# Performance work log

Hardware: AMD Instinct MI355X
Metric: run time of the kernel (lower is better)

## Reference

```python
import jax, jax.numpy as jnp
jax.config.update("jax_enable_x64", True)  # hash needs int64 wraparound semantics like torch
import numpy as np

HASH_BITS = 19
HASH_SIZE = 1 << HASH_BITS   # 2**hash_size entries
CELL_SIZE = 1.0
DIM = 8                      # feature dimensions
N = 8_388_608                # number of query positions


def _bitmix_hash(ix, iy):
    """Murmur-inspired bit-mix hash, int64 wraparound arithmetic (matches torch .long())."""
    h = ix
    h = h ^ (h >> 16)
    h = h * jnp.int64(2246822507)
    h = h ^ (h >> 13)
    h = h + iy * jnp.int64(3266489909)
    h = h ^ (h >> 16)
    return jnp.mod(h, HASH_SIZE)  # nonneg result, same as torch/python %


def setup_inputs() -> dict:
    key = jax.random.key(0)
    k1, k2 = jax.random.split(key)
    positions = jax.random.uniform(k1, (N, 2), dtype=jnp.float32, minval=0.0, maxval=4096.0)
    # dense materialization of the lazily-inserted ParameterDict: randn * 0.01 init
    table = jax.random.normal(k2, (HASH_SIZE, DIM), dtype=jnp.float32) * 0.01
    return {"positions": positions, "table": table}


def reference(positions, table):
    # quantize to integer grid cells
    ix = jnp.floor(positions[:, 0] / CELL_SIZE).astype(jnp.int64)
    iy = jnp.floor(positions[:, 1] / CELL_SIZE).astype(jnp.int64)
    idx = _bitmix_hash(ix, iy)          # [N] in [0, HASH_SIZE)
    return jnp.take(table, idx, axis=0)  # [N, DIM] gather
```

## Files before the change

kernel.cpp:

```cpp
#include <hip/hip_runtime.h>
#include <stdint.h>

#define HASH_BITS 19
#define HASH_SIZE (1u << HASH_BITS)

#define SLICE_BITS 3
#define NSLICE (1 << SLICE_BITS)
#define SLICE_SHIFT (HASH_BITS - SLICE_BITS)

#define BLOCK 256
#define IPT 8
#define CHUNK (BLOCK * IPT)

typedef float vfloat2 __attribute__((ext_vector_type(2)));
typedef float vfloat4 __attribute__((ext_vector_type(4)));

__device__ __forceinline__ uint32_t bitmix_hash(float qx, float qy) {
    uint64_t ix = (uint64_t)(uint32_t)qx;
    uint64_t iy = (uint64_t)(uint32_t)qy;
    uint64_t hh = ix;
    hh ^= hh >> 16;
    hh *= 2246822507ull;
    hh ^= hh >> 13;
    hh += iy * 3266489909ull;
    hh ^= hh >> 16;
    return (uint32_t)hh & (HASH_SIZE - 1);
}

__global__ __launch_bounds__(BLOCK) void hashgrid2d_phased(
    const vfloat2* __restrict__ pos,
    const vfloat4* __restrict__ table,
    vfloat4* __restrict__ out,
    int n, int nchunks)
{
    __shared__ vfloat4 vals[CHUNK * 2];
    const int t = threadIdx.x;

    for (int c = blockIdx.x; c < nchunks; c += gridDim.x) {
        const long long base = (long long)c * CHUNK;

        uint32_t idx[IPT];
#pragma unroll
        for (int j = 0; j < IPT; ++j) {
            long long g = base + j * BLOCK + t;
            if (g < n) {
                vfloat2 q = __builtin_nontemporal_load(&pos[g]);
                idx[j] = bitmix_hash(q.x, q.y);
            } else {
                idx[j] = 0xFFFFFFFFu;
            }
        }

        __syncthreads();

#pragma unroll 1
        for (uint32_t s = 0; s < NSLICE; ++s) {
#pragma unroll
            for (int j = 0; j < IPT; ++j) {
                if ((idx[j] >> SLICE_SHIFT) == s) {
                    size_t e = (size_t)idx[j] * 2;
                    vfloat4 lo = table[e];
                    vfloat4 hi = table[e + 1];
                    int li = j * BLOCK + t;
                    vals[li * 2]     = lo;
                    vals[li * 2 + 1] = hi;
                }
            }
        }

        __syncthreads();

#pragma unroll
        for (int k = 0; k < IPT * 2; ++k) {
            int f = k * BLOCK + t;
            long long item = base + (f >> 1);
            if (item < n)
                __builtin_nontemporal_store(vals[f], &out[base * 2 + f]);
        }
    }
}

extern "C" void kernel_launch(void* const* d_in, const int* in_sizes, int n_in,
                              void* d_out, int out_size, void* d_ws, size_t ws_size,
                              hipStream_t stream) {
    const vfloat2* pos   = (const vfloat2*)d_in[0];
    const vfloat4* table = (const vfloat4*)d_in[1];
    vfloat4* out         = (vfloat4*)d_out;

    int n = in_sizes[0] / 2;
    int nchunks = (int)(((long long)n + CHUNK - 1) / CHUNK);
    int grid = nchunks < 512 ? nchunks : 512;
    hashgrid2d_phased<<<grid, BLOCK, 0, stream>>>(pos, table, out, n, nchunks);
}
```

Before: 495.5 us.

## Split into bucketing pass and per-slice gather pass via workspace records

Replaces the single phased kernel with two kernels. The first hashes positions and uses ballot-based counting sort to write packed (local id, hash index) records grouped by table slice per 8K-item group. The second launches one block per (group, slice) so that concurrently running blocks touch limited table regions. The aim is better cache locality for the random table gather. In exchange it adds a workspace round trip for the records, a second launch, scattered output stores, and a fallback kernel for when the workspace is too small.

```diff
diff --git a/kernel.cpp b/kernel.cpp
--- a/kernel.cpp
+++ b/kernel.cpp
@@ -3,14 +3,13 @@
 
 #define HASH_BITS 19
 #define HASH_SIZE (1u << HASH_BITS)
+#define SLICE_SHIFT (HASH_BITS - 3)
+#define NSLICE 8
 
-#define SLICE_BITS 3
-#define NSLICE (1 << SLICE_BITS)
-#define SLICE_SHIFT (HASH_BITS - SLICE_BITS)
-
+#define GROUP_BITS 13
+#define GROUP (1 << GROUP_BITS)
 #define BLOCK 256
-#define IPT 8
-#define CHUNK (BLOCK * IPT)
+#define IPT (GROUP / BLOCK)
 
 typedef float vfloat2 __attribute__((ext_vector_type(2)));
 typedef float vfloat4 __attribute__((ext_vector_type(4)));
@@ -27,56 +26,124 @@
     return (uint32_t)hh & (HASH_SIZE - 1);
 }
 
-__global__ __launch_bounds__(BLOCK) void hashgrid2d_phased(
+__global__ __launch_bounds__(BLOCK) void bucket_kernel(
+    const vfloat2* __restrict__ pos,
+    uint32_t* __restrict__ records,
+    uint32_t* __restrict__ hdr,
+    long long n)
+{
+    __shared__ uint32_t cnt[BLOCK / 64][NSLICE];
+    __shared__ uint32_t scan[BLOCK / 64][NSLICE];
+    const int g = blockIdx.x;
+    const long long gbase = (long long)g << GROUP_BITS;
+    const int tid = threadIdx.x;
+    const int w = tid >> 6;
+    const int lane = tid & 63;
+    const uint64_t lt_mask = (lane == 63) ? ~0ull >> 1 : ((1ull << (lane + 1)) >> 1) - 0;
+    const uint64_t lt = (lane == 0) ? 0ull : (~0ull >> (64 - lane));
+    (void)lt_mask;
+
+    uint32_t idx[IPT];
+#pragma unroll
+    for (int j = 0; j < IPT; ++j) {
+        long long item = gbase + j * BLOCK + tid;
+        if (item < n) {
+            vfloat2 q = __builtin_nontemporal_load(&pos[item]);
+            idx[j] = bitmix_hash(q.x, q.y);
+        } else {
+            idx[j] = 0xFFFFFFFFu;
+        }
+    }
+
+    uint32_t c[NSLICE] = {0, 0, 0, 0, 0, 0, 0, 0};
+#pragma unroll
+    for (int j = 0; j < IPT; ++j) {
+        uint32_t sl = idx[j] >> SLICE_SHIFT;
+#pragma unroll
+        for (uint32_t s0 = 0; s0 < NSLICE; ++s0)
+            c[s0] += (uint32_t)__popcll(__ballot(sl == s0));
+    }
+    if (lane == 0) {
+#pragma unroll
+        for (int s0 = 0; s0 < NSLICE; ++s0) cnt[w][s0] = c[s0];
+    }
+    __syncthreads();
+
+    if (tid == 0) {
+        uint32_t run = 0;
+        for (int s0 = 0; s0 < NSLICE; ++s0) {
+            hdr[(size_t)g * NSLICE + s0] = run;
+            for (int w0 = 0; w0 < BLOCK / 64; ++w0) {
+                scan[w0][s0] = run;
+                run += cnt[w0][s0];
+            }
+        }
+    }
+    __syncthreads();
+
+    uint32_t off[NSLICE];
+#pragma unroll
+    for (int s0 = 0; s0 < NSLICE; ++s0) off[s0] = scan[w][s0];
+
+#pragma unroll
+    for (int j = 0; j < IPT; ++j) {
+        uint32_t sl = idx[j] >> SLICE_SHIFT;
+        uint32_t lid = (uint32_t)(j * BLOCK + tid);
+#pragma unroll
+        for (uint32_t s0 = 0; s0 < NSLICE; ++s0) {
+            uint64_t m = __ballot(sl == s0);
+            if (sl == s0) {
+                uint32_t rank = (uint32_t)__popcll(m & lt);
+                records[gbase + off[s0] + rank] = (lid << HASH_BITS) | idx[j];
+            }
+            off[s0] += (uint32_t)__popcll(m);
+        }
+    }
+}
+
+__global__ __launch_bounds__(BLOCK) void gather_kernel(
+    const uint32_t* __restrict__ records,
+    const uint32_t* __restrict__ hdr,
+    const vfloat4* __restrict__ table,
+    vfloat4* __restrict__ out,
+    long long n)
+{
+    const uint32_t s = blockIdx.x & (NSLICE - 1);
+    const uint32_t g = blockIdx.x >> 3;
+    const long long gbase = (long long)g << GROUP_BITS;
+    long long rem = n - gbase;
+    uint32_t gvalid = rem >= GROUP ? (uint32_t)GROUP : (uint32_t)rem;
+    uint32_t b = hdr[(size_t)g * NSLICE + s];
+    uint32_t e = (s == NSLICE - 1) ? gvalid : hdr[(size_t)g * NSLICE + s + 1];
+
+    for (uint32_t i = threadIdx.x + b; i < e; i += BLOCK) {
+        uint32_t rec = __builtin_nontemporal_load(&records[gbase + i]);
+        uint32_t id = rec & (HASH_SIZE - 1);
+        uint32_t lid = rec >> HASH_BITS;
+        vfloat4 lo = table[(size_t)id * 2];
+        vfloat4 hi = table[(size_t)id * 2 + 1];
+        size_t o = (size_t)(gbase + lid) * 2;
+        __builtin_nontemporal_store(lo, &out[o]);
+        __builtin_nontemporal_store(hi, &out[o + 1]);
+    }
+}
+
+__global__ __launch_bounds__(256) void hashgrid2d_fallback(
     const vfloat2* __restrict__ pos,
     const vfloat4* __restrict__ table,
     vfloat4* __restrict__ out,
-    int n, int nchunks)
+    long long n)
 {
-    __shared__ vfloat4 vals[CHUNK * 2];
-    const int t = threadIdx.x;
-
-    for (int c = blockIdx.x; c < nchunks; c += gridDim.x) {
-        const long long base = (long long)c * CHUNK;
-
-        uint32_t idx[IPT];
-#pragma unroll
-        for (int j = 0; j < IPT; ++j) {
-            long long g = base + j * BLOCK + t;
-            if (g < n) {
-                vfloat2 q = __builtin_nontemporal_load(&pos[g]);
-                idx[j] = bitmix_hash(q.x, q.y);
-            } else {
-                idx[j] = 0xFFFFFFFFu;
-            }
-        }
-
-        __syncthreads();
-
-#pragma unroll 1
-        for (uint32_t s = 0; s < NSLICE; ++s) {
-#pragma unroll
-            for (int j = 0; j < IPT; ++j) {
-                if ((idx[j] >> SLICE_SHIFT) == s) {
-                    size_t e = (size_t)idx[j] * 2;
-                    vfloat4 lo = table[e];
-                    vfloat4 hi = table[e + 1];
-                    int li = j * BLOCK + t;
-                    vals[li * 2]     = lo;
-                    vals[li * 2 + 1] = hi;
-                }
-            }
-        }
-
-        __syncthreads();
-
-#pragma unroll
-        for (int k = 0; k < IPT * 2; ++k) {
-            int f = k * BLOCK + t;
-            long long item = base + (f >> 1);
-            if (item < n)
-                __builtin_nontemporal_store(vals[f], &out[base * 2 + f]);
-        }
+    long long t = (long long)blockIdx.x * blockDim.x + threadIdx.x;
+    long long nitems = 2LL * n;
+    long long stride = (long long)gridDim.x * blockDim.x;
+    for (; t < nitems; t += stride) {
+        long long p = t >> 1;
+        int h = (int)(t & 1);
+        vfloat2 q = __builtin_nontemporal_load(&pos[p]);
+        uint32_t id = bitmix_hash(q.x, q.y);
+        vfloat4 vv = table[(size_t)id * 2 + h];
+        __builtin_nontemporal_store(vv, &out[(size_t)p * 2 + h]);
     }
 }
 
@@ -87,8 +154,24 @@
     const vfloat4* table = (const vfloat4*)d_in[1];
     vfloat4* out         = (vfloat4*)d_out;
 
-    int n = in_sizes[0] / 2;
-    int nchunks = (int)(((long long)n + CHUNK - 1) / CHUNK);
-    int grid = nchunks < 512 ? nchunks : 512;
-    hashgrid2d_phased<<<grid, BLOCK, 0, stream>>>(pos, table, out, n, nchunks);
+    long long n = in_sizes[0] / 2;
+    if (n <= 0) return;
+
+    long long ngroups = (n + GROUP - 1) >> GROUP_BITS;
+    size_t need = (size_t)n * 4 + (size_t)ngroups * NSLICE * 4;
+
+    if (ws_size >= need && ngroups <= 0x7FFFFFFFLL / NSLICE) {
+        uint32_t* records = (uint32_t*)d_ws;
+        uint32_t* hdr     = (uint32_t*)((char*)d_ws + (size_t)n * 4);
+
+        bucket_kernel<<<(int)ngroups, BLOCK, 0, stream>>>(pos, records, hdr, n);
+        gather_kernel<<<(int)(ngroups * NSLICE), BLOCK, 0, stream>>>(
+            records, hdr, table, out, n);
+    } else {
+        long long nitems = 2LL * n;
+        int block = 256;
+        long long needb = (nitems + block - 1) / block;
+        int grid = (int)(needb < 2048 ? needb : 2048);
+        hashgrid2d_fallback<<<grid, block, 0, stream>>>(pos, table, out, n);
+    }
 }
```

Result: slower. 852.5 us (+72.1%).
